# Performance work log

Hardware: AMD Instinct MI355X
Metric: run time of the kernel (lower is better)

Reference implementation:

```python
import jax, jax.numpy as jnp
import numpy as np


def setup_inputs() -> dict:
    key = jax.random.key(0)
    k_in, k_idx, k_neg, k_w, k_b = jax.random.split(key, 5)
    N, C_in, C_out, K, L = 8, 128, 256, 7, 16384
    x = jax.random.normal(k_in, (N, C_in, L), dtype=jnp.float32)
    idx = jax.random.randint(k_idx, (K, L), 0, L, dtype=jnp.int64)
    drop = jax.random.uniform(k_neg, (K, L)) < 0.05
    idx = jnp.where(drop, -1, idx)
    stdv = 1.0 / np.sqrt(C_in * K)
    weight = jax.random.uniform(k_w, (C_out, C_in, K), dtype=jnp.float32, minval=-stdv, maxval=stdv)
    bias = jax.random.uniform(k_b, (C_out,), dtype=jnp.float32, minval=-stdv, maxval=stdv)
    return {"input": x, "indices": idx, "weight": weight, "bias": bias}


def reference(input, indices, weight, bias):
    # indices: (K, L); -1 means zero-padding (matches utils.prepare_mask)
    mask = (indices >= 0).astype(input.dtype)          # (K, L)
    safe_idx = jnp.where(indices >= 0, indices, 0)     # (K, L)
    # im2col gather: (N, C_in, K, L), masked where neighbor is absent
    col = input[..., safe_idx] * mask
    # weight (C_out, C_in, K) contracted against col -> (N, C_out, L), mirrors bmm
    out = jnp.einsum('nckl,ock->nol', col, weight)
    out = out + bias[None, :, None]
    return out
```

## Files before the change

kernel.cpp:

```cpp
#include <hip/hip_runtime.h>
#include <stdint.h>

#define NB 8
#define CI 128
#define CO 256
#define KS 7
#define LL 16384
#define CK (CI * KS)

typedef _Float16 half8 __attribute__((ext_vector_type(8)));
typedef _Float16 half2v __attribute__((ext_vector_type(2)));
typedef float floatx4 __attribute__((ext_vector_type(4)));
typedef uint32_t uintx4 __attribute__((ext_vector_type(4)));

__device__ __forceinline__ void load16_to_lds(const void* g, void* l) {
    __builtin_amdgcn_global_load_lds(
        (const __attribute__((address_space(1))) void*)g,
        (__attribute__((address_space(3))) void*)l, 16, 0, 0);
}

__global__ __launch_bounds__(256) void convert_x(const float* __restrict__ x,
                                                 _Float16* __restrict__ xT) {
    __shared__ uint32_t tile[64][65];
    const int n  = blockIdx.y;
    const int l0 = blockIdx.x * 64;
    const int t  = threadIdx.x;
    const float* xs = x + (size_t)n * CI * LL + l0;

    const int l4  = (t & 15) * 4;
    const int cpr = t >> 4;
    #pragma unroll
    for (int p = 0; p < 4; ++p) {
        const int cp = cpr + p * 16;
        const float4 a4 = *(const float4*)(xs + (size_t)(2 * cp) * LL + l4);
        const float4 b4 = *(const float4*)(xs + (size_t)(2 * cp + 1) * LL + l4);
        half2v h;
        h[0] = (_Float16)a4.x; h[1] = (_Float16)b4.x;
        tile[l4 + 0][cp] = __builtin_bit_cast(uint32_t, h);
        h[0] = (_Float16)a4.y; h[1] = (_Float16)b4.y;
        tile[l4 + 1][cp] = __builtin_bit_cast(uint32_t, h);
        h[0] = (_Float16)a4.z; h[1] = (_Float16)b4.z;
        tile[l4 + 2][cp] = __builtin_bit_cast(uint32_t, h);
        h[0] = (_Float16)a4.w; h[1] = (_Float16)b4.w;
        tile[l4 + 3][cp] = __builtin_bit_cast(uint32_t, h);
    }
    __syncthreads();

    const int lw  = t >> 4;
    const int cp0 = (t & 15) * 4;
    _Float16* xd = xT + (size_t)n * LL * CI + (size_t)l0 * CI;
    #pragma unroll
    for (int p = 0; p < 4; ++p) {
        const int l = lw + p * 16;
        uintx4 d;
        d[0] = tile[l][cp0 + 0];
        d[1] = tile[l][cp0 + 1];
        d[2] = tile[l][cp0 + 2];
        d[3] = tile[l][cp0 + 3];
        *(uintx4*)(xd + (size_t)l * CI + cp0 * 2) = d;
    }
}

__global__ __launch_bounds__(256) void convert_w(const float* __restrict__ w,
                                                 _Float16* __restrict__ wT) {
    const int t = blockIdx.x * 256 + threadIdx.x;
    if (t >= CO * CK + 128) return;
    if (t >= CO * CK) { wT[t] = (_Float16)0.f; return; }
    const int o = t / CK;
    const int r = t - o * CK;
    const int k = r >> 7;
    const int c = r & 127;
    wT[t] = (_Float16)w[(size_t)o * CK + c * KS + k];
}

__global__ __launch_bounds__(256) void iconv_mfma(
    const _Float16* __restrict__ xT,
    const int*      __restrict__ idx,
    const _Float16* __restrict__ wT,
    const float*    __restrict__ bias,
    const _Float16* __restrict__ zrow,
    float*          __restrict__ out)
{
    __shared__ _Float16 a_lds[128 * 64];
    __shared__ _Float16 b_lds[128 * 64];

    const int l0 = blockIdx.x * 128;
    const int o0 = blockIdx.y * 128;
    const int n  = blockIdx.z;
    const int t  = threadIdx.x;
    const int lane = t & 63;
    const int wv = t >> 6;
    const int wo = (wv >> 1) * 64;
    const int wl = (wv & 1) * 64;
    const int m16 = lane & 15;
    const int q8  = (lane >> 4) * 8;

    floatx4 acc[4][4];
    #pragma unroll
    for (int i = 0; i < 4; ++i)
        #pragma unroll
        for (int j = 0; j < 4; ++j) acc[i][j] = (floatx4)0.f;

    const int srow = t >> 3;
    const int part = t & 7;

    int iv[KS][4];
    #pragma unroll
    for (int k = 0; k < KS; ++k)
        #pragma unroll
        for (int i = 0; i < 4; ++i)
            iv[k][i] = idx[k * LL + l0 + i * 32 + srow];

    const _Float16* xbase = xT + (size_t)n * LL * CI;
    const _Float16* wbase = wT + (size_t)(o0 + srow) * CK + part * 8;
    const int dst = srow * 64 + part * 8;

    for (int k = 0; k < KS; ++k) {
        for (int c0 = 0; c0 < CI; c0 += 64) {
            __syncthreads();
            #pragma unroll
            for (int i = 0; i < 4; ++i) {
                const int ii = iv[k][i];
                const _Float16* bs = (ii >= 0)
                    ? (xbase + (size_t)ii * CI + c0 + part * 8)
                    : (zrow + c0 + part * 8);
                load16_to_lds(bs, b_lds + i * 2048 + dst);
                load16_to_lds(wbase + (size_t)i * 32 * CK + k * CI + c0,
                              a_lds + i * 2048 + dst);
            }
            __syncthreads();

            #pragma unroll
            for (int kk = 0; kk < 2; ++kk) {
                half8 af[4], bf[4];
                #pragma unroll
                for (int mf = 0; mf < 4; ++mf)
                    af[mf] = *(const half8*)(a_lds + (wo + mf * 16 + m16) * 64 + kk * 32 + q8);
                #pragma unroll
                for (int nf = 0; nf < 4; ++nf)
                    bf[nf] = *(const half8*)(b_lds + (wl + nf * 16 + m16) * 64 + kk * 32 + q8);
                #pragma unroll
                for (int mf = 0; mf < 4; ++mf)
                    #pragma unroll
                    for (int nf = 0; nf < 4; ++nf)
                        acc[mf][nf] = __builtin_amdgcn_mfma_f32_16x16x32_f16(
                            af[mf], bf[nf], acc[mf][nf], 0, 0, 0);
            }
        }
    }

    const int r4 = (lane >> 4) * 4;
    #pragma unroll
    for (int mf = 0; mf < 4; ++mf) {
        const int obase = o0 + wo + mf * 16 + r4;
        const floatx4 b4 = *(const floatx4*)(bias + obase);
        #pragma unroll
        for (int nf = 0; nf < 4; ++nf) {
            const int l = l0 + wl + nf * 16 + m16;
            float* op = out + ((size_t)n * CO + obase) * LL + l;
            #pragma unroll
            for (int r = 0; r < 4; ++r)
                op[(size_t)r * LL] = acc[mf][nf][r] + b4[r];
        }
    }
}

__global__ __launch_bounds__(256) void iconv_fallback(
    const float* __restrict__ x, const int* __restrict__ idx,
    const float* __restrict__ w, const float* __restrict__ bias,
    float* __restrict__ out)
{
    __shared__ float col[CI][64];
    const int n  = blockIdx.y;
    const int l0 = blockIdx.x * 64;
    const int t  = threadIdx.x;
    const int ot = t & 63, lt = t >> 6;
    const int j = t >> 2, part = t & 3;
    float acc[4][16];
    #pragma unroll
    for (int oo = 0; oo < 4; ++oo) {
        const float bv = bias[ot * 4 + oo];
        #pragma unroll
        for (int ll = 0; ll < 16; ++ll) acc[oo][ll] = bv;
    }
    for (int k = 0; k < KS; ++k) {
        __syncthreads();
        const int i = idx[k * LL + l0 + j];
        const float* xr = x + (size_t)n * CI * LL;
        for (int q = 0; q < 32; ++q) {
            const int c = part * 32 + q;
            col[c][j] = (i >= 0) ? xr[(size_t)c * LL + i] : 0.f;
        }
        __syncthreads();
        for (int c = 0; c < CI; ++c) {
            const float* bv = &col[c][lt * 16];
            float wv[4];
            #pragma unroll
            for (int oo = 0; oo < 4; ++oo)
                wv[oo] = w[(size_t)(ot * 4 + oo) * CK + c * KS + k];
            #pragma unroll
            for (int oo = 0; oo < 4; ++oo)
                #pragma unroll
                for (int ll = 0; ll < 16; ++ll)
                    acc[oo][ll] += wv[oo] * bv[ll];
        }
    }
    #pragma unroll
    for (int oo = 0; oo < 4; ++oo) {
        float* orow = out + ((size_t)n * CO + (ot * 4 + oo)) * LL + l0 + lt * 16;
        #pragma unroll
        for (int q = 0; q < 16; ++q) orow[q] = acc[oo][q];
    }
}

extern "C" void kernel_launch(void* const* d_in, const int* in_sizes, int n_in,
                              void* d_out, int out_size, void* d_ws, size_t ws_size,
                              hipStream_t stream) {
    const float* x    = (const float*)d_in[0];
    const int*   idx  = (const int*)d_in[1];
    const float* w    = (const float*)d_in[2];
    const float* bias = (const float*)d_in[3];
    float* out = (float*)d_out;

    const size_t xt_bytes = (size_t)NB * LL * CI * sizeof(_Float16);
    const size_t wt_elems = (size_t)CO * CK + 128;
    const size_t need = xt_bytes + wt_elems * sizeof(_Float16);

    if (ws_size >= need) {
        _Float16* xT = (_Float16*)d_ws;
        _Float16* wT = (_Float16*)((char*)d_ws + xt_bytes);
        const _Float16* zr = wT + (size_t)CO * CK;
        convert_x<<<dim3(LL / 64, NB), 256, 0, stream>>>(x, xT);
        convert_w<<<dim3(((int)wt_elems + 255) / 256), 256, 0, stream>>>(w, wT);
        iconv_mfma<<<dim3(LL / 128, CO / 128, NB), 256, 0, stream>>>(
            xT, idx, wT, bias, zr, out);
    } else {
        iconv_fallback<<<dim3(LL / 64, NB), 256, 0, stream>>>(x, idx, w, bias, out);
    }
}
```

Baseline: 261.8 us.

## Merge prep kernels and use 32-wide K tiles with XOR-swizzled LDS

Fuses the x and w conversion kernels into one launch, and the weight transpose now goes through LDS with vectorized half8 stores. The MFMA kernel's K-step shrinks from 64 to 32, which halves LDS use and may allow more resident blocks. The 16-byte chunks in each LDS row are XOR-swizzled to reduce bank conflicts on fragment reads. The cost is twice as many barrier/load rounds per output tile, and each staging round issues fewer loads, which exposes more latency.

```diff
diff --git a/kernel.cpp b/kernel.cpp
--- a/kernel.cpp
+++ b/kernel.cpp
@@ -19,58 +19,68 @@
         (__attribute__((address_space(3))) void*)l, 16, 0, 0);
 }
 
-__global__ __launch_bounds__(256) void convert_x(const float* __restrict__ x,
-                                                 _Float16* __restrict__ xT) {
-    __shared__ uint32_t tile[64][65];
-    const int n  = blockIdx.y;
-    const int l0 = blockIdx.x * 64;
-    const int t  = threadIdx.x;
-    const float* xs = x + (size_t)n * CI * LL + l0;
-
-    const int l4  = (t & 15) * 4;
-    const int cpr = t >> 4;
-    #pragma unroll
-    for (int p = 0; p < 4; ++p) {
-        const int cp = cpr + p * 16;
-        const float4 a4 = *(const float4*)(xs + (size_t)(2 * cp) * LL + l4);
-        const float4 b4 = *(const float4*)(xs + (size_t)(2 * cp + 1) * LL + l4);
-        half2v h;
-        h[0] = (_Float16)a4.x; h[1] = (_Float16)b4.x;
-        tile[l4 + 0][cp] = __builtin_bit_cast(uint32_t, h);
-        h[0] = (_Float16)a4.y; h[1] = (_Float16)b4.y;
-        tile[l4 + 1][cp] = __builtin_bit_cast(uint32_t, h);
-        h[0] = (_Float16)a4.z; h[1] = (_Float16)b4.z;
-        tile[l4 + 2][cp] = __builtin_bit_cast(uint32_t, h);
-        h[0] = (_Float16)a4.w; h[1] = (_Float16)b4.w;
-        tile[l4 + 3][cp] = __builtin_bit_cast(uint32_t, h);
-    }
-    __syncthreads();
-
-    const int lw  = t >> 4;
-    const int cp0 = (t & 15) * 4;
-    _Float16* xd = xT + (size_t)n * LL * CI + (size_t)l0 * CI;
-    #pragma unroll
-    for (int p = 0; p < 4; ++p) {
-        const int l = lw + p * 16;
-        uintx4 d;
-        d[0] = tile[l][cp0 + 0];
-        d[1] = tile[l][cp0 + 1];
-        d[2] = tile[l][cp0 + 2];
-        d[3] = tile[l][cp0 + 3];
-        *(uintx4*)(xd + (size_t)l * CI + cp0 * 2) = d;
-    }
-}
-
-__global__ __launch_bounds__(256) void convert_w(const float* __restrict__ w,
-                                                 _Float16* __restrict__ wT) {
-    const int t = blockIdx.x * 256 + threadIdx.x;
-    if (t >= CO * CK + 128) return;
-    if (t >= CO * CK) { wT[t] = (_Float16)0.f; return; }
-    const int o = t / CK;
-    const int r = t - o * CK;
-    const int k = r >> 7;
-    const int c = r & 127;
-    wT[t] = (_Float16)w[(size_t)o * CK + c * KS + k];
+__global__ __launch_bounds__(256) void prep(const float* __restrict__ x,
+                                            const float* __restrict__ w,
+                                            _Float16* __restrict__ xT,
+                                            _Float16* __restrict__ wT) {
+    __shared__ uint32_t smem[64][65];
+    const int b = blockIdx.x;
+    const int t = threadIdx.x;
+
+    if (b < NB * 256) {
+        const int n  = b >> 8;
+        const int l0 = (b & 255) * 64;
+        const float* xs = x + (size_t)n * CI * LL + l0;
+        const int l4  = (t & 15) * 4;
+        const int cpr = t >> 4;
+        #pragma unroll
+        for (int p = 0; p < 4; ++p) {
+            const int cp = cpr + p * 16;
+            const float4 a4 = *(const float4*)(xs + (size_t)(2 * cp) * LL + l4);
+            const float4 b4 = *(const float4*)(xs + (size_t)(2 * cp + 1) * LL + l4);
+            half2v h;
+            h[0] = (_Float16)a4.x; h[1] = (_Float16)b4.x;
+            smem[l4 + 0][cp] = __builtin_bit_cast(uint32_t, h);
+            h[0] = (_Float16)a4.y; h[1] = (_Float16)b4.y;
+            smem[l4 + 1][cp] = __builtin_bit_cast(uint32_t, h);
+            h[0] = (_Float16)a4.z; h[1] = (_Float16)b4.z;
+            smem[l4 + 2][cp] = __builtin_bit_cast(uint32_t, h);
+            h[0] = (_Float16)a4.w; h[1] = (_Float16)b4.w;
+            smem[l4 + 3][cp] = __builtin_bit_cast(uint32_t, h);
+        }
+        __syncthreads();
+        const int lw  = t >> 4;
+        const int cp0 = (t & 15) * 4;
+        _Float16* xd = xT + (size_t)n * LL * CI + (size_t)l0 * CI;
+        #pragma unroll
+        for (int p = 0; p < 4; ++p) {
+            const int l = lw + p * 16;
+            uintx4 d;
+            d[0] = smem[l][cp0 + 0];
+            d[1] = smem[l][cp0 + 1];
+            d[2] = smem[l][cp0 + 2];
+            d[3] = smem[l][cp0 + 3];
+            *(uintx4*)(xd + (size_t)l * CI + cp0 * 2) = d;
+        }
+    } else if (b < NB * 256 + CO) {
+        const int o = b - NB * 256;
+        float* lds = (float*)smem;
+        for (int i = t; i < CK; i += 256) lds[i] = w[(size_t)o * CK + i];
+        __syncthreads();
+        if (t < CK / 8) {
+            half8 h;
+            #pragma unroll
+            for (int q = 0; q < 8; ++q) {
+                const int dd = t * 8 + q;
+                const int k = dd >> 7;
+                const int c = dd & 127;
+                h[q] = (_Float16)lds[c * KS + k];
+            }
+            *(half8*)(wT + (size_t)o * CK + t * 8) = h;
+        }
+    } else {
+        if (t < 128) wT[(size_t)CO * CK + t] = (_Float16)0.f;
+    }
 }
 
 __global__ __launch_bounds__(256) void iconv_mfma(
@@ -81,8 +91,8 @@
     const _Float16* __restrict__ zrow,
     float*          __restrict__ out)
 {
-    __shared__ _Float16 a_lds[128 * 64];
-    __shared__ _Float16 b_lds[128 * 64];
+    __shared__ _Float16 a_lds[128 * 32];
+    __shared__ _Float16 b_lds[128 * 32];
 
     const int l0 = blockIdx.x * 128;
     const int o0 = blockIdx.y * 128;
@@ -93,7 +103,7 @@
     const int wo = (wv >> 1) * 64;
     const int wl = (wv & 1) * 64;
     const int m16 = lane & 15;
-    const int q8  = (lane >> 4) * 8;
+    const int sw = ((lane >> 4) ^ ((lane >> 1) & 3)) * 8;
 
     floatx4 acc[4][4];
     #pragma unroll
@@ -101,51 +111,47 @@
         #pragma unroll
         for (int j = 0; j < 4; ++j) acc[i][j] = (floatx4)0.f;
 
-    const int srow = t >> 3;
-    const int part = t & 7;
-
-    int iv[KS][4];
-    #pragma unroll
-    for (int k = 0; k < KS; ++k)
-        #pragma unroll
-        for (int i = 0; i < 4; ++i)
-            iv[k][i] = idx[k * LL + l0 + i * 32 + srow];
-
-    const _Float16* xbase = xT + (size_t)n * LL * CI;
-    const _Float16* wbase = wT + (size_t)(o0 + srow) * CK + part * 8;
-    const int dst = srow * 64 + part * 8;
-
+    const int srow = t >> 2;
+    const int jq   = (t & 3) ^ ((t >> 3) & 3);
+
+    int iv0[KS], iv1[KS];
+    #pragma unroll
     for (int k = 0; k < KS; ++k) {
-        for (int c0 = 0; c0 < CI; c0 += 64) {
+        iv0[k] = idx[k * LL + l0 + srow];
+        iv1[k] = idx[k * LL + l0 + 64 + srow];
+    }
+
+    const _Float16* xbase  = xT + (size_t)n * LL * CI;
+    const _Float16* abase0 = wT + (size_t)(o0 + srow) * CK + jq * 8;
+    const _Float16* abase1 = wT + (size_t)(o0 + 64 + srow) * CK + jq * 8;
+
+    for (int k = 0; k < KS; ++k) {
+        const int i0 = iv0[k], i1 = iv1[k];
+        const _Float16* b0 = ((i0 >= 0) ? xbase + (size_t)i0 * CI : zrow) + jq * 8;
+        const _Float16* b1 = ((i1 >= 0) ? xbase + (size_t)i1 * CI : zrow) + jq * 8;
+        const _Float16* a0 = abase0 + k * CI;
+        const _Float16* a1 = abase1 + k * CI;
+        for (int c0 = 0; c0 < CI; c0 += 32) {
             __syncthreads();
-            #pragma unroll
-            for (int i = 0; i < 4; ++i) {
-                const int ii = iv[k][i];
-                const _Float16* bs = (ii >= 0)
-                    ? (xbase + (size_t)ii * CI + c0 + part * 8)
-                    : (zrow + c0 + part * 8);
-                load16_to_lds(bs, b_lds + i * 2048 + dst);
-                load16_to_lds(wbase + (size_t)i * 32 * CK + k * CI + c0,
-                              a_lds + i * 2048 + dst);
-            }
+            load16_to_lds(b0 + c0, b_lds + t * 8);
+            load16_to_lds(b1 + c0, b_lds + (256 + t) * 8);
+            load16_to_lds(a0 + c0, a_lds + t * 8);
+            load16_to_lds(a1 + c0, a_lds + (256 + t) * 8);
             __syncthreads();
 
-            #pragma unroll
-            for (int kk = 0; kk < 2; ++kk) {
-                half8 af[4], bf[4];
-                #pragma unroll
-                for (int mf = 0; mf < 4; ++mf)
-                    af[mf] = *(const half8*)(a_lds + (wo + mf * 16 + m16) * 64 + kk * 32 + q8);
+            half8 af[4], bf[4];
+            #pragma unroll
+            for (int mf = 0; mf < 4; ++mf)
+                af[mf] = *(const half8*)(a_lds + (wo + mf * 16 + m16) * 32 + sw);
+            #pragma unroll
+            for (int nf = 0; nf < 4; ++nf)
+                bf[nf] = *(const half8*)(b_lds + (wl + nf * 16 + m16) * 32 + sw);
+            #pragma unroll
+            for (int mf = 0; mf < 4; ++mf)
                 #pragma unroll
                 for (int nf = 0; nf < 4; ++nf)
-                    bf[nf] = *(const half8*)(b_lds + (wl + nf * 16 + m16) * 64 + kk * 32 + q8);
-                #pragma unroll
-                for (int mf = 0; mf < 4; ++mf)
-                    #pragma unroll
-                    for (int nf = 0; nf < 4; ++nf)
-                        acc[mf][nf] = __builtin_amdgcn_mfma_f32_16x16x32_f16(
-                            af[mf], bf[nf], acc[mf][nf], 0, 0, 0);
-            }
+                    acc[mf][nf] = __builtin_amdgcn_mfma_f32_16x16x32_f16(
+                        af[mf], bf[nf], acc[mf][nf], 0, 0, 0);
         }
     }
 
@@ -230,8 +236,7 @@
         _Float16* xT = (_Float16*)d_ws;
         _Float16* wT = (_Float16*)((char*)d_ws + xt_bytes);
         const _Float16* zr = wT + (size_t)CO * CK;
-        convert_x<<<dim3(LL / 64, NB), 256, 0, stream>>>(x, xT);
-        convert_w<<<dim3(((int)wt_elems + 255) / 256), 256, 0, stream>>>(w, wT);
+        prep<<<dim3(NB * 256 + CO + 1), 256, 0, stream>>>(x, w, xT, wT);
         iconv_mfma<<<dim3(LL / 128, CO / 128, NB), 256, 0, stream>>>(
             xT, idx, wT, bias, zr, out);
     } else {
```

New measurement: 264.0 us. Within noise of the previous version (+0.8%).
